# Kernel optimization log

Measured on AMD Instinct MI355X. Metric: run time of the kernel, lower is better.

The kernel has to match this reference:

```python
import jax, jax.numpy as jnp
import numpy as np
import math

INNER = 96
EPS = 1e-8  # torch CosineSimilarity eps


def _proj(x, W1, W2):
    # nn.Linear(C,C,bias=False) -> ReLU -> nn.Linear(C,inner,bias=False)
    return jax.nn.relu(x @ W1) @ W2


def _cos(a, b):
    # torch CosineSimilarity(dim=-1): dot / (max(||a||,eps)*max(||b||,eps))
    num = jnp.sum(a * b, axis=-1)
    na = jnp.maximum(jnp.linalg.norm(a, axis=-1), EPS)
    nb = jnp.maximum(jnp.linalg.norm(b, axis=-1), EPS)
    return num / (na * nb)


def setup_inputs() -> dict:
    key = jax.random.key(0)
    ks = jax.random.split(key, 8)
    B, C, H, W = 128, 768, 7, 7
    sc1 = 1.0 / math.sqrt(C)
    inp = {
        "features_a": jax.random.normal(ks[0], (B, C, H, W), jnp.float32),
        "features_b": jax.random.normal(ks[1], (B, C, H, W), jnp.float32),
        "Wq1": jax.random.normal(ks[2], (C, C), jnp.float32) * sc1,
        "Wq2": jax.random.normal(ks[3], (C, INNER), jnp.float32) * sc1,
        "Wk1": jax.random.normal(ks[4], (C, C), jnp.float32) * sc1,
        "Wk2": jax.random.normal(ks[5], (C, INNER), jnp.float32) * sc1,
        "Wv1": jax.random.normal(ks[6], (C, C), jnp.float32) * sc1,
        "Wv2": jax.random.normal(ks[7], (C, INNER), jnp.float32) * sc1,
    }
    return inp


def reference(features_a, features_b, Wq1, Wq2, Wk1, Wk2, Wv1, Wv2):
    B, C = features_a.shape[0], features_a.shape[1]
    # [B, C, H, W] -> [B, S, C]
    fa = features_a.reshape(B, C, -1).transpose(0, 2, 1)
    fb = features_b.reshape(features_b.shape[0], C, -1).transpose(0, 2, 1)

    qa, ka, va = _proj(fa, Wq1, Wq2), _proj(fa, Wk1, Wk2), _proj(fa, Wv1, Wv2)
    qb, kb, vb = _proj(fb, Wq1, Wq2), _proj(fb, Wk1, Wk2), _proj(fb, Wv1, Wv2)

    scale = 1.0 / math.sqrt(INNER)

    # query_b vs key_a: [Bb, Ba, Sq, Sk]
    scores_ba = jnp.einsum('bqe,ake->baqk', qb, ka) * scale
    probs_ba = jax.nn.softmax(scores_ba, axis=-1)
    aligned_a = jnp.einsum('baqk,ake->baqe', probs_ba, va)  # [Bb, Ba, S, inner]

    # query_a vs key_b: [Bb, Ba, Sq, Sk]
    scores_ab = jnp.einsum('aqe,bke->baqk', qa, kb) * scale
    probs_ab = jax.nn.softmax(scores_ab, axis=-1)
    aligned_b = jnp.einsum('baqk,bke->baqe', probs_ab, vb)  # [Bb, Ba, S, inner]

    sim = _cos(va[None, :, :, :], aligned_b) + _cos(vb[:, None, :, :], aligned_a)
    return sim.mean(-1)  # [Bb, Ba]
```

## Files before the change

kernel.cpp:

```cpp
#include <hip/hip_runtime.h>
#include <hip/hip_bf16.h>
#include <math.h>

typedef __attribute__((ext_vector_type(8))) short bf16x8;
typedef __attribute__((ext_vector_type(4))) float f32x4;

#define MROWS 12544
#define CDIM 768
#define INNER 96
#define S49 49
#define NSIDE 6272
#define SCALE 0.10206207261596577f
#define SCALE_EXP2 ((float)(0.10206207261596577 * 1.4426950408889634))

__device__ __forceinline__ unsigned short f2bf(float f) {
  union { float f; unsigned u; } v; v.f = f;
  unsigned u = v.u;
  return (unsigned short)((u + 0x7fffu + ((u >> 16) & 1u)) >> 16);
}
__device__ __forceinline__ float bf2f(unsigned short h) {
  union { unsigned u; float f; } v; v.u = ((unsigned)h) << 16;
  return v.f;
}
__device__ __forceinline__ unsigned pack_bf16_rn(float a, float b) {
  union { float f; unsigned u; } ua, ub; ua.f = a; ub.f = b;
  return __builtin_amdgcn_perm(ub.u + 0x8000u, ua.u + 0x8000u, 0x07060302u);
}

__device__ __forceinline__ void gld16(const unsigned short* g, unsigned short* l) {
  __builtin_amdgcn_global_load_lds(
      (const __attribute__((address_space(1))) unsigned int*)(g),
      (__attribute__((address_space(3))) unsigned int*)(l), 16, 0, 0);
}

__global__ __launch_bounds__(256) void prep_all(
    const float* __restrict__ fa, const float* __restrict__ fb,
    const float* __restrict__ w10, const float* __restrict__ w11,
    const float* __restrict__ w12, const float* __restrict__ w20,
    const float* __restrict__ w21, const float* __restrict__ w22,
    unsigned short* __restrict__ X,
    unsigned short* __restrict__ W1T, unsigned short* __restrict__ W2T,
    unsigned short* __restrict__ VtKpad) {
  const int t = threadIdx.x;
  int id = blockIdx.x;
  if (id < 3072) {
    __shared__ float T[64][50];
    const int z = id / 1536; id -= z * 1536;
    const int ct = id % 12, img = id / 12;
    const float* feat = z ? fb : fa;
    const float* src = feat + (size_t)img * (CDIM * S49) + (size_t)ct * 64 * S49;
    for (int idx = t; idx < 64 * S49; idx += 256) {
      int cc = idx / S49, s = idx - cc * S49;
      T[cc][s] = src[cc * S49 + s];
    }
    __syncthreads();
    unsigned short* dst = X + (size_t)(z * 128 + img) * S49 * CDIM + ct * 64;
    for (int idx = t; idx < S49 * 64; idx += 256) {
      int s = idx >> 6, cc = idx & 63;
      dst[(size_t)s * CDIM + cc] = f2bf(T[cc][s]);
    }
  } else if (id < 5016) {
    __shared__ float T[32][33];
    id -= 3072;
    const float* src;
    unsigned short* dst;
    int C, ctile, rtile;
    if (id < 1728) {
      int wdx = id / 576, tid = id - wdx * 576;
      ctile = tid % 24; rtile = tid / 24;
      src = wdx == 0 ? w10 : (wdx == 1 ? w11 : w12);
      dst = W1T + (size_t)wdx * CDIM * CDIM;
      C = CDIM;
    } else {
      id -= 1728;
      int wdx = id / 72, tid = id - wdx * 72;
      ctile = tid % 3; rtile = tid / 3;
      src = wdx == 0 ? w20 : (wdx == 1 ? w21 : w22);
      dst = W2T + (size_t)wdx * INNER * CDIM;
      C = INNER;
    }
    const int c0 = ctile * 32, r0 = rtile * 32;
    for (int idx = t; idx < 1024; idx += 256) {
      int rr = idx >> 5, cc = idx & 31;
      T[rr][cc] = src[(size_t)(r0 + rr) * C + c0 + cc];
    }
    __syncthreads();
    for (int idx = t; idx < 1024; idx += 256) {
      int rr = idx >> 5, cc = idx & 31;
      dst[(size_t)(c0 + rr) * CDIM + r0 + cc] = f2bf(T[cc][rr]);
    }
  } else {
    id -= 5016;
    ushort4* p4 = (ushort4*)VtKpad;
    const ushort4 z = make_ushort4(0, 0, 0, 0);
#pragma unroll
    for (int i = 0; i < 32; i++)
      p4[(size_t)id * 8192 + i * 256 + t] = z;
  }
}

__global__ __launch_bounds__(512) void gemm1b4(const unsigned short* __restrict__ X,
                                               const unsigned short* __restrict__ W1T,
                                               unsigned short* __restrict__ H,
                                               int wbase, int hsel) {
  __shared__ __align__(16) unsigned short As[128 * 64];
  __shared__ __align__(16) unsigned short Bs[128 * 64];
  const int t = threadIdx.x;
  const int lane = t & 63, w = t >> 6;
  const int lr = lane & 15, lq = lane >> 4;
  const int wm = w & 3;
  const int wn = w >> 2;
  const int m0 = blockIdx.y * 128, n0 = blockIdx.x * 128;
  const int wdx = blockIdx.z + wbase;
  const unsigned short* W1w = W1T + (size_t)wdx * CDIM * CDIM;
  unsigned short* Hw = H + (hsel ? (size_t)wdx * MROWS * CDIM : 0);
  const f32x4 z4 = {0.f, 0.f, 0.f, 0.f};
  f32x4 acc[2][4] = {{z4, z4, z4, z4}, {z4, z4, z4, z4}};

  for (int k0 = 0; k0 < CDIM; k0 += 64) {
    __syncthreads();
#pragma unroll
    for (int j = 0; j < 2; j++) {
      int idx = t + j * 512;
      int row = idx >> 3, col = (idx & 7) * 8;
      gld16(X + (size_t)(m0 + row) * CDIM + k0 + col, As + idx * 8);
      gld16(W1w + (size_t)(n0 + row) * CDIM + k0 + col, Bs + idx * 8);
    }
    __syncthreads();
#pragma unroll
    for (int ks = 0; ks < 2; ks++) {
      bf16x8 a[2], b[4];
#pragma unroll
      for (int mt = 0; mt < 2; mt++)
        a[mt] = *(const bf16x8*)(As + (wm * 32 + mt * 16 + lr) * 64 + ks * 32 + lq * 8);
#pragma unroll
      for (int nt = 0; nt < 4; nt++)
        b[nt] = *(const bf16x8*)(Bs + (wn * 64 + nt * 16 + lr) * 64 + ks * 32 + lq * 8);
#pragma unroll
      for (int mt = 0; mt < 2; mt++)
#pragma unroll
        for (int nt = 0; nt < 4; nt++)
          acc[mt][nt] = __builtin_amdgcn_mfma_f32_16x16x32_bf16(a[mt], b[nt], acc[mt][nt], 0, 0, 0);
    }
  }
#pragma unroll
  for (int mt = 0; mt < 2; mt++)
#pragma unroll
    for (int nt = 0; nt < 4; nt++)
#pragma unroll
      for (int r = 0; r < 4; r++) {
        int m = m0 + wm * 32 + mt * 16 + lq * 4 + r;
        int n = n0 + wn * 64 + nt * 16 + lr;
        Hw[(size_t)m * CDIM + n] = f2bf(fmaxf(acc[mt][nt][r], 0.f));
      }
}

#define LDK 72
__global__ __launch_bounds__(256) void gemm2b3(const unsigned short* __restrict__ H,
                                               const unsigned short* __restrict__ W2T,
                                               unsigned short* __restrict__ QKV,
                                               unsigned short* __restrict__ Kpad,
                                               unsigned short* __restrict__ Vt,
                                               float* __restrict__ vnorm,
                                               int wbase, int hsel) {
  __shared__ __align__(16) unsigned short As[64 * LDK];
  __shared__ __align__(16) unsigned short Bs[96 * LDK];
  const int t = threadIdx.x;
  const int lane = t & 63, w = t >> 6;
  const int lr = lane & 15, lq = lane >> 4;
  const int m0 = blockIdx.x * 64;
  const int wdx = blockIdx.y + wbase;
  const unsigned short* Hw = H + (hsel ? (size_t)wdx * MROWS * CDIM : 0);
  const unsigned short* W2w = W2T + (size_t)wdx * INNER * CDIM;
  const f32x4 z4 = {0.f, 0.f, 0.f, 0.f};
  f32x4 acc[6] = {z4, z4, z4, z4, z4, z4};

  for (int k0 = 0; k0 < CDIM; k0 += 64) {
    __syncthreads();
    for (int c = t; c < 512; c += 256) {
      int r = c >> 3, kc = (c & 7) * 8;
      *(uint4*)(As + r * LDK + kc) = *(const uint4*)(Hw + (size_t)(m0 + r) * CDIM + k0 + kc);
    }
    for (int c = t; c < 768; c += 256) {
      int r = c >> 3, kc = (c & 7) * 8;
      *(uint4*)(Bs + r * LDK + kc) = *(const uint4*)(W2w + (size_t)r * CDIM + k0 + kc);
    }
    __syncthreads();
#pragma unroll
    for (int kk = 0; kk < 2; kk++) {
      bf16x8 a = *(const bf16x8*)(As + (w * 16 + lr) * LDK + kk * 32 + lq * 8);
#pragma unroll
      for (int nt = 0; nt < 6; nt++) {
        bf16x8 b = *(const bf16x8*)(Bs + (nt * 16 + lr) * LDK + kk * 32 + lq * 8);
        acc[nt] = __builtin_amdgcn_mfma_f32_16x16x32_bf16(a, b, acc[nt], 0, 0, 0);
      }
    }
  }
  float nsq[4] = {0.f, 0.f, 0.f, 0.f};
#pragma unroll
  for (int nt = 0; nt < 6; nt++)
#pragma unroll
    for (int r = 0; r < 4; r++) {
      int m = m0 + w * 16 + lq * 4 + r;
      int e = nt * 16 + lr;
      float v = acc[nt][r];
      int img = m / 49, s = m - img * 49;
      if (wdx == 0) {
        QKV[(size_t)m * INNER + e] = f2bf(v * SCALE_EXP2);
      } else if (wdx == 1) {
        Kpad[(size_t)(img * 64 + s) * INNER + e] = f2bf(v);
      } else {
        QKV[(size_t)(2 * MROWS + m) * INNER + e] = f2bf(v);
        Vt[(size_t)img * (INNER * 64) + e * 64 + s] = f2bf(v);
        nsq[r] += v * v;
      }
    }
  if (wdx == 2) {
#pragma unroll
    for (int r = 0; r < 4; r++) {
      float p = nsq[r];
      p += __shfl_xor(p, 1, 16);
      p += __shfl_xor(p, 2, 16);
      p += __shfl_xor(p, 4, 16);
      p += __shfl_xor(p, 8, 16);
      if (lr == 0) vnorm[m0 + w * 16 + lq * 4 + r] = sqrtf(p);
    }
  }
}

__global__ __launch_bounds__(256) void attn11(const unsigned short* __restrict__ Qp,
                                              const unsigned short* __restrict__ Kpad,
                                              const unsigned short* __restrict__ V,
                                              const unsigned short* __restrict__ Vt,
                                              const float* __restrict__ vnorm,
                                              float* __restrict__ cosbuf) {
  __shared__ __align__(16) unsigned short Ks[64 * INNER];
  __shared__ __align__(16) unsigned short VtS[INNER * 64];
  __shared__ __align__(16) unsigned short Ps[4][32 * 64];

  const int t = threadIdx.x;
  const int lane = t & 63, w = t >> 6;
  const int lr = lane & 15, lq = lane >> 4;
  const f32x4 z4 = {0.f, 0.f, 0.f, 0.f};

  int bx = blockIdx.x;
  const int dir = bx / 784; bx -= dir * 784;
  const int chunk = bx >> 4, fg = bx & 15;
  const int r0 = chunk * 128;
  const int qbase = dir * NSIDE;

  int goK[3], goV[3], lo[3];
#pragma unroll
  for (int j = 0; j < 3; j++) {
    int l = (w * 3 + j) * 64 + lane;
    lo[j] = l * 8;
    int rK = l / 12, scK = l - rK * 12;
    int ccK = scK - ((rK >> 1) & 7); if (ccK < 0) ccK += 12;
    goK[j] = rK * INNER + ccK * 8;
    int rV = l >> 3, scV = l & 7;
    int ccV = (scV - (rV & 7)) & 7;
    goV[j] = rV * 64 + ccV * 8;
  }
  int rdK[3], rdV[2];
#pragma unroll
  for (int ks = 0; ks < 3; ks++) {
    int sc = (ks * 4 + lq + ((lr >> 1) & 7)) % 12;
    rdK[ks] = lr * INNER + sc * 8;
  }
#pragma unroll
  for (int ks = 0; ks < 2; ks++) {
    int sc = (ks * 4 + lq + (lr & 7)) & 7;
    rdV[ks] = lr * 64 + sc * 8;
  }

  bf16x8 qf[2][3];
#pragma unroll
  for (int qt = 0; qt < 2; qt++) {
    const int qrow = qbase + r0 + w * 32 + qt * 16 + lr;
#pragma unroll
    for (int ks = 0; ks < 3; ks++)
      qf[qt][ks] = *(const bf16x8*)(Qp + (size_t)qrow * INNER + ks * 32 + lq * 8);
  }
  float rv[2][6][4], invvn[2];
#pragma unroll
  for (int qt = 0; qt < 2; qt++) {
    const int qrow = qbase + r0 + w * 32 + qt * 16 + lr;
    invvn[qt] = 1.f / fmaxf(vnorm[qrow], 1e-8f);
#pragma unroll
    for (int et = 0; et < 6; et++) {
      ushort4 u = *(const ushort4*)(V + (size_t)qrow * INNER + et * 16 + lq * 4);
      rv[qt][et][0] = bf2f(u.x); rv[qt][et][1] = bf2f(u.y);
      rv[qt][et][2] = bf2f(u.z); rv[qt][et][3] = bf2f(u.w);
    }
  }

  unsigned short* Pw = &Ps[w][0];
  const int kimg0 = (dir == 0 ? 128 : 0) + fg * 8;
  {
    const unsigned short* kg = Kpad + (size_t)kimg0 * (64 * INNER);
#pragma unroll
    for (int j = 0; j < 3; j++) gld16(kg + goK[j], Ks + lo[j]);
  }
  for (int fi = 0; fi < 8; fi++) {
    const int f = fg * 8 + fi;
    __syncthreads();
    {
      const unsigned short* vg = Vt + (size_t)(kimg0 + fi) * (INNER * 64);
#pragma unroll
      for (int j = 0; j < 3; j++) gld16(vg + goV[j], VtS + lo[j]);
    }
    f32x4 s4[2][4] = {{z4, z4, z4, z4}, {z4, z4, z4, z4}};
    __builtin_amdgcn_s_setprio(1);
#pragma unroll
    for (int ks = 0; ks < 3; ks++) {
#pragma unroll
      for (int kt = 0; kt < 4; kt++) {
        bf16x8 a = *(const bf16x8*)(Ks + kt * (16 * INNER) + rdK[ks]);
        s4[0][kt] = __builtin_amdgcn_mfma_f32_16x16x32_bf16(a, qf[0][ks], s4[0][kt], 0, 0, 0);
        s4[1][kt] = __builtin_amdgcn_mfma_f32_16x16x32_bf16(a, qf[1][ks], s4[1][kt], 0, 0, 0);
      }
    }
    __builtin_amdgcn_s_setprio(0);
#pragma unroll
    for (int qt = 0; qt < 2; qt++)
#pragma unroll
      for (int kt = 0; kt < 4; kt++) {
        float e0 = __builtin_exp2f(s4[qt][kt][0]);
        float e1 = __builtin_exp2f(s4[qt][kt][1]);
        float e2 = __builtin_exp2f(s4[qt][kt][2]);
        float e3 = __builtin_exp2f(s4[qt][kt][3]);
        uint2 pk = make_uint2(pack_bf16_rn(e0, e1), pack_bf16_rn(e2, e3));
        int row = qt * 16 + lr;
        int ch = (2 * kt + (lq >> 1)) ^ (row & 7);
        *(uint2*)(Pw + row * 64 + ch * 8 + (lq & 1) * 4) = pk;
      }
    __syncthreads();
    if (fi < 7) {
      const unsigned short* kg = Kpad + (size_t)(kimg0 + fi + 1) * (64 * INNER);
#pragma unroll
      for (int j = 0; j < 3; j++) gld16(kg + goK[j], Ks + lo[j]);
    }
    f32x4 pv[2][6] = {{z4, z4, z4, z4, z4, z4}, {z4, z4, z4, z4, z4, z4}};
    __builtin_amdgcn_s_setprio(1);
#pragma unroll
    for (int ks = 0; ks < 2; ks++) {
      int row0 = 0 * 16 + lr, row1 = 1 * 16 + lr;
      int ch0 = ((ks * 4 + lq) ^ (row0 & 7));
      int ch1 = ((ks * 4 + lq) ^ (row1 & 7));
      bf16x8 b0 = *(const bf16x8*)(Pw + row0 * 64 + ch0 * 8);
      bf16x8 b1 = *(const bf16x8*)(Pw + row1 * 64 + ch1 * 8);
#pragma unroll
      for (int et = 0; et < 6; et++) {
        bf16x8 a = *(const bf16x8*)(VtS + et * (16 * 64) + rdV[ks]);
        pv[0][et] = __builtin_amdgcn_mfma_f32_16x16x32_bf16(a, b0, pv[0][et], 0, 0, 0);
        pv[1][et] = __builtin_amdgcn_mfma_f32_16x16x32_bf16(a, b1, pv[1][et], 0, 0, 0);
      }
    }
    __builtin_amdgcn_s_setprio(0);
#pragma unroll
    for (int qt = 0; qt < 2; qt++) {
      float d = 0.f, nn = 0.f;
#pragma unroll
      for (int et = 0; et < 6; et++)
#pragma unroll
        for (int r = 0; r < 4; r++) {
          float al = pv[qt][et][r];
          d += al * rv[qt][et][r];
          nn += al * al;
        }
      d += __shfl_xor(d, 16, 64);  d += __shfl_xor(d, 32, 64);
      nn += __shfl_xor(nn, 16, 64); nn += __shfl_xor(nn, 32, 64);
      if (lane < 16) {
        float cv = d * __frsqrt_rn(fmaxf(nn, 1e-40f)) * invvn[qt];
        cosbuf[(size_t)(dir * 128 + f) * NSIDE + r0 + w * 32 + qt * 16 + lr] = cv;
      }
    }
  }
}

__global__ __launch_bounds__(256) void reduce_out(const float* __restrict__ cosbuf,
                                                  float* __restrict__ out) {
  const int t = threadIdx.x, lane = t & 63, wv = t >> 6;
  const int pair = blockIdx.x * 4 + wv;
  const int bb = pair >> 7, aa = pair & 127;
  float v = 0.f;
  if (lane < S49) {
    v  = cosbuf[(size_t)bb * NSIDE + aa * S49 + lane];
    v += cosbuf[(size_t)(128 + aa) * NSIDE + bb * S49 + lane];
  }
  for (int m = 1; m < 64; m <<= 1) v += __shfl_xor(v, m, 64);
  if (lane == 0) out[pair] = v * (1.f / 49.f);
}

extern "C" void kernel_launch(void* const* d_in, const int* in_sizes, int n_in,
                              void* d_out, int out_size, void* d_ws, size_t ws_size,
                              hipStream_t stream) {
  const float* fa  = (const float*)d_in[0];
  const float* fb  = (const float*)d_in[1];
  const float* W1[3] = {(const float*)d_in[2], (const float*)d_in[4], (const float*)d_in[6]};
  const float* W2[3] = {(const float*)d_in[3], (const float*)d_in[5], (const float*)d_in[7]};
  float* out = (float*)d_out;

  unsigned short* p = (unsigned short*)d_ws;
  unsigned short* Xbf = p;                 p += (size_t)MROWS * CDIM;
  unsigned short* W1T = p;                 p += (size_t)3 * CDIM * CDIM;
  unsigned short* W2T = p;                 p += (size_t)3 * INNER * CDIM;
  unsigned short* QKV = p;                 p += (size_t)3 * MROWS * INNER;
  unsigned short* Vt  = p;                 p += (size_t)256 * INNER * 64;
  unsigned short* Kpad = p;                p += (size_t)256 * 64 * INNER;
  float* vnorm = (float*)p;                p += (size_t)MROWS * 2;
  float* cosbuf = (float*)p;               p += (size_t)256 * NSIDE * 2;
  unsigned short* H = p;                   p += (size_t)3 * MROWS * CDIM;
  const size_t need_batched = (size_t)(p - (unsigned short*)d_ws) * 2;
  const int batched = ws_size >= need_batched;

  prep_all<<<dim3(5112), 256, 0, stream>>>(fa, fb, W1[0], W1[1], W1[2],
                                           W2[0], W2[1], W2[2],
                                           Xbf, W1T, W2T, Vt );
  if (batched) {
    gemm1b4<<<dim3(CDIM / 128, MROWS / 128, 3), 512, 0, stream>>>(Xbf, W1T, H, 0, 1);
    gemm2b3<<<dim3(MROWS / 64, 3), 256, 0, stream>>>(H, W2T, QKV, Kpad, Vt, vnorm, 0, 1);
  } else {
    for (int wdx = 0; wdx < 3; wdx++) {
      gemm1b4<<<dim3(CDIM / 128, MROWS / 128, 1), 512, 0, stream>>>(Xbf, W1T, H, wdx, 0);
      gemm2b3<<<dim3(MROWS / 64, 1), 256, 0, stream>>>(H, W2T, QKV, Kpad, Vt, vnorm, wdx, 0);
    }
  }
  attn11<<<dim3(2 * 784), 256, 0, stream>>>(
      QKV, Kpad, QKV + (size_t)2 * MROWS * INNER, Vt, vnorm, cosbuf);
  reduce_out<<<dim3(4096), 256, 0, stream>>>(cosbuf, out);
}
```

Baseline: 301.8 us.

## Double-buffer K tiles in LDS and read V fragments directly from global

The attention kernel now keeps two LDS buffers for K. The next image's K tile is prefetched at the top of each iteration, which removes the second barrier per iteration. The V^T tile is no longer staged through LDS; each lane loads its MFMA operand straight from global memory (served by L1/L2 cache). This trades LDS staging and synchronization for uncached-latency global loads inside the PV MFMA loop. Note that the top barrier must now cover reuse of the P buffer across iterations.

After: 341.8 us. +13.3%, slower.

```diff
diff --git a/kernel.cpp b/kernel.cpp
--- a/kernel.cpp
+++ b/kernel.cpp
@@ -228,14 +228,13 @@
   }
 }
 
-__global__ __launch_bounds__(256) void attn11(const unsigned short* __restrict__ Qp,
+__global__ __launch_bounds__(256) void attn12(const unsigned short* __restrict__ Qp,
                                               const unsigned short* __restrict__ Kpad,
                                               const unsigned short* __restrict__ V,
                                               const unsigned short* __restrict__ Vt,
                                               const float* __restrict__ vnorm,
                                               float* __restrict__ cosbuf) {
-  __shared__ __align__(16) unsigned short Ks[64 * INNER];
-  __shared__ __align__(16) unsigned short VtS[INNER * 64];
+  __shared__ __align__(16) unsigned short KsD[2][64 * INNER];
   __shared__ __align__(16) unsigned short Ps[4][32 * 64];
 
   const int t = threadIdx.x;
@@ -249,7 +248,7 @@
   const int r0 = chunk * 128;
   const int qbase = dir * NSIDE;
 
-  int goK[3], goV[3], lo[3];
+  int goK[3], lo[3];
 #pragma unroll
   for (int j = 0; j < 3; j++) {
     int l = (w * 3 + j) * 64 + lane;
@@ -257,20 +256,12 @@
     int rK = l / 12, scK = l - rK * 12;
     int ccK = scK - ((rK >> 1) & 7); if (ccK < 0) ccK += 12;
     goK[j] = rK * INNER + ccK * 8;
-    int rV = l >> 3, scV = l & 7;
-    int ccV = (scV - (rV & 7)) & 7;
-    goV[j] = rV * 64 + ccV * 8;
-  }
-  int rdK[3], rdV[2];
+  }
+  int rdK[3];
 #pragma unroll
   for (int ks = 0; ks < 3; ks++) {
     int sc = (ks * 4 + lq + ((lr >> 1) & 7)) % 12;
     rdK[ks] = lr * INNER + sc * 8;
-  }
-#pragma unroll
-  for (int ks = 0; ks < 2; ks++) {
-    int sc = (ks * 4 + lq + (lr & 7)) & 7;
-    rdV[ks] = lr * 64 + sc * 8;
   }
 
   bf16x8 qf[2][3];
@@ -296,26 +287,30 @@
 
   unsigned short* Pw = &Ps[w][0];
   const int kimg0 = (dir == 0 ? 128 : 0) + fg * 8;
+  const unsigned short* vbase = Vt + (size_t)kimg0 * (INNER * 64) + lr * 64 + lq * 8;
+
   {
     const unsigned short* kg = Kpad + (size_t)kimg0 * (64 * INNER);
 #pragma unroll
-    for (int j = 0; j < 3; j++) gld16(kg + goK[j], Ks + lo[j]);
+    for (int j = 0; j < 3; j++) gld16(kg + goK[j], &KsD[0][0] + lo[j]);
   }
   for (int fi = 0; fi < 8; fi++) {
     const int f = fg * 8 + fi;
     __syncthreads();
-    {
-      const unsigned short* vg = Vt + (size_t)(kimg0 + fi) * (INNER * 64);
-#pragma unroll
-      for (int j = 0; j < 3; j++) gld16(vg + goV[j], VtS + lo[j]);
-    }
+    if (fi < 7) {
+      const unsigned short* kg = Kpad + (size_t)(kimg0 + fi + 1) * (64 * INNER);
+      unsigned short* kd = &KsD[1 - (fi & 1)][0];
+#pragma unroll
+      for (int j = 0; j < 3; j++) gld16(kg + goK[j], kd + lo[j]);
+    }
+    const unsigned short* KsC = &KsD[fi & 1][0];
     f32x4 s4[2][4] = {{z4, z4, z4, z4}, {z4, z4, z4, z4}};
     __builtin_amdgcn_s_setprio(1);
 #pragma unroll
     for (int ks = 0; ks < 3; ks++) {
 #pragma unroll
       for (int kt = 0; kt < 4; kt++) {
-        bf16x8 a = *(const bf16x8*)(Ks + kt * (16 * INNER) + rdK[ks]);
+        bf16x8 a = *(const bf16x8*)(KsC + kt * (16 * INNER) + rdK[ks]);
         s4[0][kt] = __builtin_amdgcn_mfma_f32_16x16x32_bf16(a, qf[0][ks], s4[0][kt], 0, 0, 0);
         s4[1][kt] = __builtin_amdgcn_mfma_f32_16x16x32_bf16(a, qf[1][ks], s4[1][kt], 0, 0, 0);
       }
@@ -334,12 +329,7 @@
         int ch = (2 * kt + (lq >> 1)) ^ (row & 7);
         *(uint2*)(Pw + row * 64 + ch * 8 + (lq & 1) * 4) = pk;
       }
-    __syncthreads();
-    if (fi < 7) {
-      const unsigned short* kg = Kpad + (size_t)(kimg0 + fi + 1) * (64 * INNER);
-#pragma unroll
-      for (int j = 0; j < 3; j++) gld16(kg + goK[j], Ks + lo[j]);
-    }
+    const unsigned short* vg = vbase + (size_t)fi * (INNER * 64);
     f32x4 pv[2][6] = {{z4, z4, z4, z4, z4, z4}, {z4, z4, z4, z4, z4, z4}};
     __builtin_amdgcn_s_setprio(1);
 #pragma unroll
@@ -351,7 +341,7 @@
       bf16x8 b1 = *(const bf16x8*)(Pw + row1 * 64 + ch1 * 8);
 #pragma unroll
       for (int et = 0; et < 6; et++) {
-        bf16x8 a = *(const bf16x8*)(VtS + et * (16 * 64) + rdV[ks]);
+        bf16x8 a = *(const bf16x8*)(vg + et * 1024 + ks * 32);
         pv[0][et] = __builtin_amdgcn_mfma_f32_16x16x32_bf16(a, b0, pv[0][et], 0, 0, 0);
         pv[1][et] = __builtin_amdgcn_mfma_f32_16x16x32_bf16(a, b1, pv[1][et], 0, 0, 0);
       }
@@ -426,7 +416,7 @@
       gemm2b3<<<dim3(MROWS / 64, 1), 256, 0, stream>>>(H, W2T, QKV, Kpad, Vt, vnorm, wdx, 0);
     }
   }
-  attn11<<<dim3(2 * 784), 256, 0, stream>>>(
+  attn12<<<dim3(2 * 784), 256, 0, stream>>>(
       QKV, Kpad, QKV + (size_t)2 * MROWS * INNER, Vt, vnorm, cosbuf);
   reduce_out<<<dim3(4096), 256, 0, stream>>>(cosbuf, out);
 }
```

## Fuse two-layer projection GEMMs into one kernel keeping hidden tile in LDS

Applied to the files above, without the earlier changes.

Replaces the separate first-layer GEMM (which wrote the ReLU hidden activations H to global memory) and the second-layer GEMM with a single kernel. Each block computes a 64-row slab of H in 128-column chunks, stores it swizzled in shared memory, and immediately multiplies it by a swizzled W2 chunk. This removes the large H write and read round trip and one launch. In exchange, each block rereads the whole W1 matrix for only 64 rows, which lowers arithmetic reuse per block, and the grid is smaller with heavier LDS use.

Result: slower. 389.0 us (+28.9%).

```diff
diff --git a/kernel.cpp b/kernel.cpp
--- a/kernel.cpp
+++ b/kernel.cpp
@@ -99,111 +99,98 @@
   }
 }
 
-__global__ __launch_bounds__(512) void gemm1b4(const unsigned short* __restrict__ X,
-                                               const unsigned short* __restrict__ W1T,
-                                               unsigned short* __restrict__ H,
-                                               int wbase, int hsel) {
-  __shared__ __align__(16) unsigned short As[128 * 64];
+__global__ __launch_bounds__(512) void gemm_fused(const unsigned short* __restrict__ X,
+                                                  const unsigned short* __restrict__ W1T,
+                                                  const unsigned short* __restrict__ W2T,
+                                                  unsigned short* __restrict__ QKV,
+                                                  unsigned short* __restrict__ Kpad,
+                                                  unsigned short* __restrict__ Vt,
+                                                  float* __restrict__ vnorm) {
+  __shared__ __align__(16) unsigned short As[64 * 64];
   __shared__ __align__(16) unsigned short Bs[128 * 64];
+  __shared__ __align__(16) unsigned short Hs[64 * 128];
+  __shared__ __align__(16) unsigned short W2s[96 * 128];
+  __shared__ float nsqp[2][64];
+
   const int t = threadIdx.x;
   const int lane = t & 63, w = t >> 6;
   const int lr = lane & 15, lq = lane >> 4;
-  const int wm = w & 3;
-  const int wn = w >> 2;
-  const int m0 = blockIdx.y * 128, n0 = blockIdx.x * 128;
-  const int wdx = blockIdx.z + wbase;
+  const int wm = w >> 1, we = w & 1;
+  const int m0 = blockIdx.x * 64;
+  const int wdx = blockIdx.y;
   const unsigned short* W1w = W1T + (size_t)wdx * CDIM * CDIM;
-  unsigned short* Hw = H + (hsel ? (size_t)wdx * MROWS * CDIM : 0);
-  const f32x4 z4 = {0.f, 0.f, 0.f, 0.f};
-  f32x4 acc[2][4] = {{z4, z4, z4, z4}, {z4, z4, z4, z4}};
-
-  for (int k0 = 0; k0 < CDIM; k0 += 64) {
-    __syncthreads();
-#pragma unroll
-    for (int j = 0; j < 2; j++) {
-      int idx = t + j * 512;
-      int row = idx >> 3, col = (idx & 7) * 8;
-      gld16(X + (size_t)(m0 + row) * CDIM + k0 + col, As + idx * 8);
-      gld16(W1w + (size_t)(n0 + row) * CDIM + k0 + col, Bs + idx * 8);
-    }
-    __syncthreads();
-#pragma unroll
-    for (int ks = 0; ks < 2; ks++) {
-      bf16x8 a[2], b[4];
-#pragma unroll
-      for (int mt = 0; mt < 2; mt++)
-        a[mt] = *(const bf16x8*)(As + (wm * 32 + mt * 16 + lr) * 64 + ks * 32 + lq * 8);
-#pragma unroll
-      for (int nt = 0; nt < 4; nt++)
-        b[nt] = *(const bf16x8*)(Bs + (wn * 64 + nt * 16 + lr) * 64 + ks * 32 + lq * 8);
-#pragma unroll
-      for (int mt = 0; mt < 2; mt++)
-#pragma unroll
-        for (int nt = 0; nt < 4; nt++)
-          acc[mt][nt] = __builtin_amdgcn_mfma_f32_16x16x32_bf16(a[mt], b[nt], acc[mt][nt], 0, 0, 0);
-    }
-  }
-#pragma unroll
-  for (int mt = 0; mt < 2; mt++)
-#pragma unroll
-    for (int nt = 0; nt < 4; nt++)
-#pragma unroll
-      for (int r = 0; r < 4; r++) {
-        int m = m0 + wm * 32 + mt * 16 + lq * 4 + r;
-        int n = n0 + wn * 64 + nt * 16 + lr;
-        Hw[(size_t)m * CDIM + n] = f2bf(fmaxf(acc[mt][nt][r], 0.f));
-      }
-}
-
-#define LDK 72
-__global__ __launch_bounds__(256) void gemm2b3(const unsigned short* __restrict__ H,
-                                               const unsigned short* __restrict__ W2T,
-                                               unsigned short* __restrict__ QKV,
-                                               unsigned short* __restrict__ Kpad,
-                                               unsigned short* __restrict__ Vt,
-                                               float* __restrict__ vnorm,
-                                               int wbase, int hsel) {
-  __shared__ __align__(16) unsigned short As[64 * LDK];
-  __shared__ __align__(16) unsigned short Bs[96 * LDK];
-  const int t = threadIdx.x;
-  const int lane = t & 63, w = t >> 6;
-  const int lr = lane & 15, lq = lane >> 4;
-  const int m0 = blockIdx.x * 64;
-  const int wdx = blockIdx.y + wbase;
-  const unsigned short* Hw = H + (hsel ? (size_t)wdx * MROWS * CDIM : 0);
   const unsigned short* W2w = W2T + (size_t)wdx * INNER * CDIM;
   const f32x4 z4 = {0.f, 0.f, 0.f, 0.f};
-  f32x4 acc[6] = {z4, z4, z4, z4, z4, z4};
-
-  for (int k0 = 0; k0 < CDIM; k0 += 64) {
-    __syncthreads();
-    for (int c = t; c < 512; c += 256) {
-      int r = c >> 3, kc = (c & 7) * 8;
-      *(uint4*)(As + r * LDK + kc) = *(const uint4*)(Hw + (size_t)(m0 + r) * CDIM + k0 + kc);
-    }
-    for (int c = t; c < 768; c += 256) {
-      int r = c >> 3, kc = (c & 7) * 8;
-      *(uint4*)(Bs + r * LDK + kc) = *(const uint4*)(W2w + (size_t)r * CDIM + k0 + kc);
-    }
-    __syncthreads();
-#pragma unroll
-    for (int kk = 0; kk < 2; kk++) {
-      bf16x8 a = *(const bf16x8*)(As + (w * 16 + lr) * LDK + kk * 32 + lq * 8);
-#pragma unroll
-      for (int nt = 0; nt < 6; nt++) {
-        bf16x8 b = *(const bf16x8*)(Bs + (nt * 16 + lr) * LDK + kk * 32 + lq * 8);
-        acc[nt] = __builtin_amdgcn_mfma_f32_16x16x32_bf16(a, b, acc[nt], 0, 0, 0);
+  f32x4 Oacc[3] = {z4, z4, z4};
+
+  for (int np = 0; np < 6; np++) {
+    __syncthreads();
+    {
+#pragma unroll
+      for (int j = 0; j < 3; j++) {
+        int l = t + j * 512;
+        int e = l >> 4, ch = l & 15;
+        gld16(W2w + (size_t)e * CDIM + np * 128 + ((ch ^ (e & 7)) * 8),
+              W2s + l * 8);
+      }
+    }
+    f32x4 Hacc[4] = {z4, z4, z4, z4};
+    for (int k0 = 0; k0 < CDIM; k0 += 64) {
+      __syncthreads();
+      {
+        int l = t;
+        int row = l >> 3, ch = l & 7;
+        gld16(X + (size_t)(m0 + row) * CDIM + k0 + ch * 8, As + l * 8);
+      }
+#pragma unroll
+      for (int j = 0; j < 2; j++) {
+        int l = t + j * 512;
+        int row = l >> 3, ch = l & 7;
+        gld16(W1w + (size_t)(np * 128 + row) * CDIM + k0 + ch * 8, Bs + l * 8);
+      }
+      __syncthreads();
+#pragma unroll
+      for (int ks = 0; ks < 2; ks++) {
+        bf16x8 a = *(const bf16x8*)(Bs + (w * 16 + lr) * 64 + ks * 32 + lq * 8);
+#pragma unroll
+        for (int mt = 0; mt < 4; mt++) {
+          bf16x8 b = *(const bf16x8*)(As + (mt * 16 + lr) * 64 + ks * 32 + lq * 8);
+          Hacc[mt] = __builtin_amdgcn_mfma_f32_16x16x32_bf16(a, b, Hacc[mt], 0, 0, 0);
+        }
+      }
+    }
+#pragma unroll
+    for (int mt = 0; mt < 4; mt++) {
+      int m = mt * 16 + lr;
+      uint2 pk = make_uint2(
+          pack_bf16_rn(fmaxf(Hacc[mt][0], 0.f), fmaxf(Hacc[mt][1], 0.f)),
+          pack_bf16_rn(fmaxf(Hacc[mt][2], 0.f), fmaxf(Hacc[mt][3], 0.f)));
+      int ch = 2 * w + (lq >> 1);
+      *(uint2*)((char*)Hs + m * 256 + ((ch ^ (m & 7)) * 16) + (lq & 1) * 8) = pk;
+    }
+    __syncthreads();
+#pragma unroll
+    for (int kt = 0; kt < 4; kt++) {
+      int am = wm * 16 + lr;
+      bf16x8 a = *(const bf16x8*)((const char*)Hs + am * 256 +
+                                  (((kt * 4 + lq) ^ (am & 7)) * 16));
+#pragma unroll
+      for (int et = 0; et < 3; et++) {
+        int e = we * 48 + et * 16 + lr;
+        bf16x8 b = *(const bf16x8*)((const char*)W2s + e * 256 +
+                                    (((kt * 4 + lq) ^ (e & 7)) * 16));
+        Oacc[et] = __builtin_amdgcn_mfma_f32_16x16x32_bf16(a, b, Oacc[et], 0, 0, 0);
       }
     }
   }
   float nsq[4] = {0.f, 0.f, 0.f, 0.f};
 #pragma unroll
-  for (int nt = 0; nt < 6; nt++)
+  for (int et = 0; et < 3; et++)
 #pragma unroll
     for (int r = 0; r < 4; r++) {
-      int m = m0 + w * 16 + lq * 4 + r;
-      int e = nt * 16 + lr;
-      float v = acc[nt][r];
+      int m = m0 + wm * 16 + lq * 4 + r;
+      int e = we * 48 + et * 16 + lr;
+      float v = Oacc[et][r];
       int img = m / 49, s = m - img * 49;
       if (wdx == 0) {
         QKV[(size_t)m * INNER + e] = f2bf(v * SCALE_EXP2);
@@ -223,8 +210,10 @@
       p += __shfl_xor(p, 2, 16);
       p += __shfl_xor(p, 4, 16);
       p += __shfl_xor(p, 8, 16);
-      if (lr == 0) vnorm[m0 + w * 16 + lq * 4 + r] = sqrtf(p);
-    }
+      if (lr == 0) nsqp[we][wm * 16 + lq * 4 + r] = p;
+    }
+    __syncthreads();
+    if (t < 64) vnorm[m0 + t] = sqrtf(nsqp[0][t] + nsqp[1][t]);
   }
 }
 
@@ -410,22 +399,12 @@
   unsigned short* Kpad = p;                p += (size_t)256 * 64 * INNER;
   float* vnorm = (float*)p;                p += (size_t)MROWS * 2;
   float* cosbuf = (float*)p;               p += (size_t)256 * NSIDE * 2;
-  unsigned short* H = p;                   p += (size_t)3 * MROWS * CDIM;
-  const size_t need_batched = (size_t)(p - (unsigned short*)d_ws) * 2;
-  const int batched = ws_size >= need_batched;
 
   prep_all<<<dim3(5112), 256, 0, stream>>>(fa, fb, W1[0], W1[1], W1[2],
                                            W2[0], W2[1], W2[2],
                                            Xbf, W1T, W2T, Vt );
-  if (batched) {
-    gemm1b4<<<dim3(CDIM / 128, MROWS / 128, 3), 512, 0, stream>>>(Xbf, W1T, H, 0, 1);
-    gemm2b3<<<dim3(MROWS / 64, 3), 256, 0, stream>>>(H, W2T, QKV, Kpad, Vt, vnorm, 0, 1);
-  } else {
-    for (int wdx = 0; wdx < 3; wdx++) {
-      gemm1b4<<<dim3(CDIM / 128, MROWS / 128, 1), 512, 0, stream>>>(Xbf, W1T, H, wdx, 0);
-      gemm2b3<<<dim3(MROWS / 64, 1), 256, 0, stream>>>(H, W2T, QKV, Kpad, Vt, vnorm, wdx, 0);
-    }
-  }
+  gemm_fused<<<dim3(MROWS / 64, 3), 512, 0, stream>>>(Xbf, W1T, W2T,
+                                                      QKV, Kpad, Vt, vnorm);
   attn11<<<dim3(2 * 784), 256, 0, stream>>>(
       QKV, Kpad, QKV + (size_t)2 * MROWS * INNER, Vt, vnorm, cosbuf);
   reduce_out<<<dim3(4096), 256, 0, stream>>>(cosbuf, out);
```
